# Kernel tuning notes

Measured on AMD Instinct MI355X. Metric: run time of the kernel, lower is better.

The kernel has to match this reference:

```python
import jax, jax.numpy as jnp
import numpy as np

B, N, F_IN, F_OUT = 16, 1024, 128, 128

def setup_inputs() -> dict:
    key = jax.random.key(0)
    k1, k2, k3 = jax.random.split(key, 3)
    X = jax.random.normal(k1, (B, N, F_IN), dtype=jnp.float32)
    A = jax.random.uniform(k2, (B, N, N), dtype=jnp.float32)
    W = jax.random.normal(k3, (F_IN, F_OUT), dtype=jnp.float32)
    return {"X": X, "A": A, "W": W}

def reference(X, A, W):
    # A_hat = A + I  (batched add of identity)
    n = A.shape[-1]
    A_hat = A + jnp.eye(n, dtype=A.dtype)  # [B,N,N]
    # D_hat^{-1/2} applied as elementwise row/col scaling (torch builds diag
    # matrices and inverts; mathematically identical for diagonal D).
    deg = jnp.sum(A_hat, axis=-1)               # [B,N]
    d_inv_sqrt = 1.0 / jnp.sqrt(deg)            # [B,N]
    A_norm = A_hat * d_inv_sqrt[:, :, None] * d_inv_sqrt[:, None, :]  # [B,N,N]
    out = jnp.einsum('bnm,bmf->bnf', A_norm, X)  # aggregation bmm
    out = jnp.einsum('bnf,fg->bng', out, W)      # weight matmul
    return out
```

## Files before the change

kernel.cpp:

```cpp
#include <hip/hip_runtime.h>

#define BATCH 16
#define NN 1024
#define FF 128

typedef __attribute__((ext_vector_type(8))) short bf16x8;
typedef __attribute__((ext_vector_type(4))) float f32x4;

__device__ __forceinline__ unsigned short f2bf(float x) {
  unsigned u = __float_as_uint(x);
  u += 0x7fff + ((u >> 16) & 1);
  return (unsigned short)(u >> 16);
}
__device__ __forceinline__ float bf2f(unsigned short b) {
  return __uint_as_float(((unsigned)b) << 16);
}

__global__ __launch_bounds__(256) void k_deg(const float* __restrict__ A,
                                             float* __restrict__ d) {
  int row  = blockIdx.x * 4 + (threadIdx.x >> 6);
  int lane = threadIdx.x & 63;
  const float4* Ar = (const float4*)(A + (size_t)row * NN);
  float s = 0.f;
#pragma unroll
  for (int i = 0; i < 4; ++i) {
    float4 v = Ar[lane + i * 64];
    s += (v.x + v.y) + (v.z + v.w);
  }
#pragma unroll
  for (int off = 32; off > 0; off >>= 1) s += __shfl_down(s, off, 64);
  if (lane == 0) d[row] = rsqrtf(s + 1.0f);
}

__global__ __launch_bounds__(256) void k_wt(const float* __restrict__ W,
                                            unsigned short* __restrict__ Wt) {
  int id = blockIdx.x * 256 + threadIdx.x;
  int g = id >> 7, f = id & 127;
  Wt[g * 128 + f] = f2bf(W[f * 128 + g]);
}

#define K2S 152
__global__ __launch_bounds__(256) void k_xw(const float* __restrict__ X,
                                            const unsigned short* __restrict__ Wt,
                                            const float* __restrict__ d,
                                            unsigned short* __restrict__ Yt) {
  __shared__ __align__(16) unsigned short Xl[64 * K2S];
  __shared__ __align__(16) unsigned short Wl[128 * K2S];
  __shared__ float dl[64];
  int b  = blockIdx.x >> 4;
  int m0 = (blockIdx.x & 15) * 64;
  int t  = threadIdx.x;

#pragma unroll
  for (int i = 0; i < 8; ++i) {
    int s = t + i * 256;
    int r = s >> 5, f4 = (s & 31) * 4;
    float4 v = *(const float4*)(X + ((size_t)(b * NN + m0 + r) * FF + f4));
    ushort4 p; p.x = f2bf(v.x); p.y = f2bf(v.y); p.z = f2bf(v.z); p.w = f2bf(v.w);
    *(ushort4*)(&Xl[r * K2S + f4]) = p;
  }
#pragma unroll
  for (int i = 0; i < 8; ++i) {
    int s = t + i * 256;
    int g = s >> 4, c8 = (s & 15) * 8;
    uint4 v = *(const uint4*)(Wt + (g * 128 + c8));
    *(uint4*)(&Wl[g * K2S + c8]) = v;
  }
  if (t < 64) dl[t] = d[b * NN + m0 + t];
  __syncthreads();

  int wave = t >> 6, lane = t & 63;
  int wr = wave >> 1, wc = wave & 1;
  int quad = lane >> 4, l16 = lane & 15;

  f32x4 acc[2][4];
#pragma unroll
  for (int mt = 0; mt < 2; ++mt)
#pragma unroll
    for (int ct = 0; ct < 4; ++ct) acc[mt][ct] = (f32x4){0.f, 0.f, 0.f, 0.f};

#pragma unroll
  for (int k0 = 0; k0 < 128; k0 += 32) {
    bf16x8 a[2], bb[4];
#pragma unroll
    for (int mt = 0; mt < 2; ++mt) {
      int m = wr * 32 + mt * 16 + l16;
      a[mt] = *(const bf16x8*)(&Xl[m * K2S + k0 + quad * 8]);
    }
#pragma unroll
    for (int ct = 0; ct < 4; ++ct) {
      int g = wc * 64 + ct * 16 + l16;
      bb[ct] = *(const bf16x8*)(&Wl[g * K2S + k0 + quad * 8]);
    }
#pragma unroll
    for (int mt = 0; mt < 2; ++mt)
#pragma unroll
      for (int ct = 0; ct < 4; ++ct)
        acc[mt][ct] = __builtin_amdgcn_mfma_f32_16x16x32_bf16(a[mt], bb[ct], acc[mt][ct], 0, 0, 0);
  }

#pragma unroll
  for (int mt = 0; mt < 2; ++mt) {
    int mb = wr * 32 + mt * 16 + quad * 4;
#pragma unroll
    for (int ct = 0; ct < 4; ++ct) {
      int g = wc * 64 + ct * 16 + l16;
      ushort4 p;
      p.x = f2bf(dl[mb + 0] * acc[mt][ct][0]);
      p.y = f2bf(dl[mb + 1] * acc[mt][ct][1]);
      p.z = f2bf(dl[mb + 2] * acc[mt][ct][2]);
      p.w = f2bf(dl[mb + 3] * acc[mt][ct][3]);
      *(ushort4*)(Yt + ((size_t)(b * 128 + g) * NN + m0 + mb)) = p;
    }
  }
}

#define K3S 56
__global__ __launch_bounds__(256) void k_agg(const float* __restrict__ A,
                                             const unsigned short* __restrict__ Yt,
                                             const float* __restrict__ d,
                                             float* __restrict__ out) {
  __shared__ __align__(16) unsigned short Al[32 * K3S];
  __shared__ __align__(16) unsigned short Yl[128 * K3S];
  int b  = blockIdx.x >> 5;
  int n0 = (blockIdx.x & 31) * 32;
  int t  = threadIdx.x;
  int wave = t >> 6, lane = t & 63;
  int wr = wave >> 1, wc = wave & 1;
  int quad = lane >> 4, l16 = lane & 15;

  int ar = t >> 3, ac4 = (t & 7) * 4;
  const float* Ap = A + ((size_t)(b * NN + n0 + ar) * NN + ac4);
  int yg0 = t >> 2,         yc0 = (t & 3) * 8;
  int yg1 = (t + 256) >> 2, yc1 = ((t + 256) & 3) * 8;
  const unsigned short* Yp0 = Yt + ((size_t)(b * 128 + yg0) * NN + yc0);
  const unsigned short* Yp1 = Yt + ((size_t)(b * 128 + yg1) * NN + yc1);

  f32x4 acc[4];
#pragma unroll
  for (int ct = 0; ct < 4; ++ct) acc[ct] = (f32x4){0.f, 0.f, 0.f, 0.f};

  float4 av = *(const float4*)(Ap);
  uint4 yv0 = *(const uint4*)(Yp0);
  uint4 yv1 = *(const uint4*)(Yp1);

  for (int k0 = 0; k0 < NN; k0 += 32) {
    __syncthreads();
    ushort4 ap; ap.x = f2bf(av.x); ap.y = f2bf(av.y); ap.z = f2bf(av.z); ap.w = f2bf(av.w);
    *(ushort4*)(&Al[ar * K3S + ac4]) = ap;
    *(uint4*)(&Yl[yg0 * K3S + yc0]) = yv0;
    *(uint4*)(&Yl[yg1 * K3S + yc1]) = yv1;
    __syncthreads();

    if (k0 + 32 < NN) {
      av  = *(const float4*)(Ap  + k0 + 32);
      yv0 = *(const uint4*)(Yp0 + k0 + 32);
      yv1 = *(const uint4*)(Yp1 + k0 + 32);
    }

    bf16x8 af = *(const bf16x8*)(&Al[(wr * 16 + l16) * K3S + quad * 8]);
#pragma unroll
    for (int ct = 0; ct < 4; ++ct) {
      bf16x8 bf = *(const bf16x8*)(&Yl[(wc * 64 + ct * 16 + l16) * K3S + quad * 8]);
      acc[ct] = __builtin_amdgcn_mfma_f32_16x16x32_bf16(af, bf, acc[ct], 0, 0, 0);
    }
  }

  int nb = n0 + wr * 16 + quad * 4;
  float4 d4 = *(const float4*)(d + b * NN + nb);
#pragma unroll
  for (int ct = 0; ct < 4; ++ct) {
    int g = wc * 64 + ct * 16 + l16;
    ushort4 yv = *(const ushort4*)(Yt + ((size_t)(b * 128 + g) * NN + nb));
    float* op = out + ((size_t)(b * NN + nb) * FF + g);
    op[0 * FF] = d4.x * (acc[ct][0] + bf2f(yv.x));
    op[1 * FF] = d4.y * (acc[ct][1] + bf2f(yv.y));
    op[2 * FF] = d4.z * (acc[ct][2] + bf2f(yv.z));
    op[3 * FF] = d4.w * (acc[ct][3] + bf2f(yv.w));
  }
}

extern "C" void kernel_launch(void* const* d_in, const int* in_sizes, int n_in,
                              void* d_out, int out_size, void* d_ws, size_t ws_size,
                              hipStream_t stream) {
  const float* X = (const float*)d_in[0];
  const float* A = (const float*)d_in[1];
  const float* W = (const float*)d_in[2];
  float* out = (float*)d_out;

  char* ws = (char*)d_ws;
  float*          dinv = (float*)ws;
  unsigned short* Wt   = (unsigned short*)(ws + 65536);
  unsigned short* Yt   = (unsigned short*)(ws + 65536 + 32768);

  k_deg<<<dim3(4096), dim3(256), 0, stream>>>(A, dinv);
  k_wt <<<dim3(64),   dim3(256), 0, stream>>>(W, Wt);
  k_xw <<<dim3(256),  dim3(256), 0, stream>>>(X, Wt, dinv, Yt);
  k_agg<<<dim3(512),  dim3(256), 0, stream>>>(A, Yt, dinv, out);
}
```

Before: 126.7 us.

## Drop LDS staging in xw and agg kernels, load MFMA fragments directly; fuse W transpose

Both matmul kernels now load MFMA operand fragments straight from global memory into registers instead of staging through shared memory with barriers. The aggregation kernel gives each wave an independent 16-row by 64-column tile with register double-buffering and no __syncthreads. The W transpose is folded into the degree kernel as extra blocks, removing one launch. The trade-off is that each wave reads A and Yt on its own without sharing through LDS, which means more redundant global/L2 traffic and less coalesced access patterns.

```diff
diff --git a/kernel.cpp b/kernel.cpp
--- a/kernel.cpp
+++ b/kernel.cpp
@@ -15,9 +15,25 @@
 __device__ __forceinline__ float bf2f(unsigned short b) {
   return __uint_as_float(((unsigned)b) << 16);
 }
+__device__ __forceinline__ bf16x8 cvt8(float4 a, float4 b) {
+  bf16x8 r;
+  r[0] = (short)f2bf(a.x); r[1] = (short)f2bf(a.y);
+  r[2] = (short)f2bf(a.z); r[3] = (short)f2bf(a.w);
+  r[4] = (short)f2bf(b.x); r[5] = (short)f2bf(b.y);
+  r[6] = (short)f2bf(b.z); r[7] = (short)f2bf(b.w);
+  return r;
+}
 
 __global__ __launch_bounds__(256) void k_deg(const float* __restrict__ A,
-                                             float* __restrict__ d) {
+                                             const float* __restrict__ W,
+                                             float* __restrict__ d,
+                                             unsigned short* __restrict__ Wt) {
+  if (blockIdx.x >= 4096) {
+    int id = (blockIdx.x - 4096) * 256 + threadIdx.x;
+    int g = id >> 7, f = id & 127;
+    Wt[g * 128 + f] = f2bf(W[f * 128 + g]);
+    return;
+  }
   int row  = blockIdx.x * 4 + (threadIdx.x >> 6);
   int lane = threadIdx.x & 63;
   const float4* Ar = (const float4*)(A + (size_t)row * NN);
@@ -32,146 +48,104 @@
   if (lane == 0) d[row] = rsqrtf(s + 1.0f);
 }
 
-__global__ __launch_bounds__(256) void k_wt(const float* __restrict__ W,
-                                            unsigned short* __restrict__ Wt) {
-  int id = blockIdx.x * 256 + threadIdx.x;
-  int g = id >> 7, f = id & 127;
-  Wt[g * 128 + f] = f2bf(W[f * 128 + g]);
-}
-
-#define K2S 152
 __global__ __launch_bounds__(256) void k_xw(const float* __restrict__ X,
                                             const unsigned short* __restrict__ Wt,
                                             const float* __restrict__ d,
                                             unsigned short* __restrict__ Yt) {
-  __shared__ __align__(16) unsigned short Xl[64 * K2S];
-  __shared__ __align__(16) unsigned short Wl[128 * K2S];
-  __shared__ float dl[64];
+  int t = threadIdx.x;
+  int wave = t >> 6, lane = t & 63;
+  int quad = lane >> 4, l16 = lane & 15;
   int b  = blockIdx.x >> 4;
-  int m0 = (blockIdx.x & 15) * 64;
-  int t  = threadIdx.x;
+  int m0 = ((blockIdx.x & 15) * 4 + wave) * 16;
 
+  const float* Xp = X + ((size_t)(b * NN + m0 + l16) * FF) + quad * 8;
+
+  f32x4 acc[8];
 #pragma unroll
-  for (int i = 0; i < 8; ++i) {
-    int s = t + i * 256;
-    int r = s >> 5, f4 = (s & 31) * 4;
-    float4 v = *(const float4*)(X + ((size_t)(b * NN + m0 + r) * FF + f4));
-    ushort4 p; p.x = f2bf(v.x); p.y = f2bf(v.y); p.z = f2bf(v.z); p.w = f2bf(v.w);
-    *(ushort4*)(&Xl[r * K2S + f4]) = p;
-  }
-#pragma unroll
-  for (int i = 0; i < 8; ++i) {
-    int s = t + i * 256;
-    int g = s >> 4, c8 = (s & 15) * 8;
-    uint4 v = *(const uint4*)(Wt + (g * 128 + c8));
-    *(uint4*)(&Wl[g * K2S + c8]) = v;
-  }
-  if (t < 64) dl[t] = d[b * NN + m0 + t];
-  __syncthreads();
-
-  int wave = t >> 6, lane = t & 63;
-  int wr = wave >> 1, wc = wave & 1;
-  int quad = lane >> 4, l16 = lane & 15;
-
-  f32x4 acc[2][4];
-#pragma unroll
-  for (int mt = 0; mt < 2; ++mt)
-#pragma unroll
-    for (int ct = 0; ct < 4; ++ct) acc[mt][ct] = (f32x4){0.f, 0.f, 0.f, 0.f};
+  for (int ct = 0; ct < 8; ++ct) acc[ct] = (f32x4){0.f, 0.f, 0.f, 0.f};
 
 #pragma unroll
   for (int k0 = 0; k0 < 128; k0 += 32) {
-    bf16x8 a[2], bb[4];
+    float4 a0 = *(const float4*)(Xp + k0);
+    float4 a1 = *(const float4*)(Xp + k0 + 4);
+    bf16x8 af = cvt8(a0, a1);
 #pragma unroll
-    for (int mt = 0; mt < 2; ++mt) {
-      int m = wr * 32 + mt * 16 + l16;
-      a[mt] = *(const bf16x8*)(&Xl[m * K2S + k0 + quad * 8]);
+    for (int ct = 0; ct < 8; ++ct) {
+      bf16x8 wf = *(const bf16x8*)(Wt + (ct * 16 + l16) * 128 + k0 + quad * 8);
+      acc[ct] = __builtin_amdgcn_mfma_f32_16x16x32_bf16(af, wf, acc[ct], 0, 0, 0);
     }
-#pragma unroll
-    for (int ct = 0; ct < 4; ++ct) {
-      int g = wc * 64 + ct * 16 + l16;
-      bb[ct] = *(const bf16x8*)(&Wl[g * K2S + k0 + quad * 8]);
-    }
-#pragma unroll
-    for (int mt = 0; mt < 2; ++mt)
-#pragma unroll
-      for (int ct = 0; ct < 4; ++ct)
-        acc[mt][ct] = __builtin_amdgcn_mfma_f32_16x16x32_bf16(a[mt], bb[ct], acc[mt][ct], 0, 0, 0);
   }
 
+  int mb = m0 + quad * 4;
+  float4 d4 = *(const float4*)(d + b * NN + mb);
 #pragma unroll
-  for (int mt = 0; mt < 2; ++mt) {
-    int mb = wr * 32 + mt * 16 + quad * 4;
-#pragma unroll
-    for (int ct = 0; ct < 4; ++ct) {
-      int g = wc * 64 + ct * 16 + l16;
-      ushort4 p;
-      p.x = f2bf(dl[mb + 0] * acc[mt][ct][0]);
-      p.y = f2bf(dl[mb + 1] * acc[mt][ct][1]);
-      p.z = f2bf(dl[mb + 2] * acc[mt][ct][2]);
-      p.w = f2bf(dl[mb + 3] * acc[mt][ct][3]);
-      *(ushort4*)(Yt + ((size_t)(b * 128 + g) * NN + m0 + mb)) = p;
-    }
+  for (int ct = 0; ct < 8; ++ct) {
+    int g = ct * 16 + l16;
+    ushort4 p;
+    p.x = f2bf(d4.x * acc[ct][0]);
+    p.y = f2bf(d4.y * acc[ct][1]);
+    p.z = f2bf(d4.z * acc[ct][2]);
+    p.w = f2bf(d4.w * acc[ct][3]);
+    *(ushort4*)(Yt + (size_t)(b * 128 + g) * NN + mb) = p;
   }
 }
 
-#define K3S 56
-__global__ __launch_bounds__(256) void k_agg(const float* __restrict__ A,
-                                             const unsigned short* __restrict__ Yt,
-                                             const float* __restrict__ d,
-                                             float* __restrict__ out) {
-  __shared__ __align__(16) unsigned short Al[32 * K3S];
-  __shared__ __align__(16) unsigned short Yl[128 * K3S];
-  int b  = blockIdx.x >> 5;
-  int n0 = (blockIdx.x & 31) * 32;
-  int t  = threadIdx.x;
+__global__ __launch_bounds__(256, 2) void k_agg(const float* __restrict__ A,
+                                                const unsigned short* __restrict__ Yt,
+                                                const float* __restrict__ d,
+                                                float* __restrict__ out) {
+  int t = threadIdx.x;
   int wave = t >> 6, lane = t & 63;
-  int wr = wave >> 1, wc = wave & 1;
   int quad = lane >> 4, l16 = lane & 15;
+  int b   = blockIdx.x >> 5;
+  int rem = blockIdx.x & 31;
+  int ntile = rem * 2 + (wave >> 1);
+  int gh    = wave & 1;
+  int n0 = ntile * 16;
+  int g0 = gh * 64;
 
-  int ar = t >> 3, ac4 = (t & 7) * 4;
-  const float* Ap = A + ((size_t)(b * NN + n0 + ar) * NN + ac4);
-  int yg0 = t >> 2,         yc0 = (t & 3) * 8;
-  int yg1 = (t + 256) >> 2, yc1 = ((t + 256) & 3) * 8;
-  const unsigned short* Yp0 = Yt + ((size_t)(b * 128 + yg0) * NN + yc0);
-  const unsigned short* Yp1 = Yt + ((size_t)(b * 128 + yg1) * NN + yc1);
+  const float* Ap = A + (size_t)(b * NN + n0 + l16) * NN + quad * 8;
+  const unsigned short* Yp[4];
+#pragma unroll
+  for (int ct = 0; ct < 4; ++ct)
+    Yp[ct] = Yt + (size_t)(b * 128 + g0 + ct * 16 + l16) * NN + quad * 8;
 
   f32x4 acc[4];
 #pragma unroll
   for (int ct = 0; ct < 4; ++ct) acc[ct] = (f32x4){0.f, 0.f, 0.f, 0.f};
 
-  float4 av = *(const float4*)(Ap);
-  uint4 yv0 = *(const uint4*)(Yp0);
-  uint4 yv1 = *(const uint4*)(Yp1);
+  float4 a0 = *(const float4*)(Ap);
+  float4 a1 = *(const float4*)(Ap + 4);
+  bf16x8 y[4];
+#pragma unroll
+  for (int ct = 0; ct < 4; ++ct) y[ct] = *(const bf16x8*)(Yp[ct]);
 
+#pragma unroll 2
   for (int k0 = 0; k0 < NN; k0 += 32) {
-    __syncthreads();
-    ushort4 ap; ap.x = f2bf(av.x); ap.y = f2bf(av.y); ap.z = f2bf(av.z); ap.w = f2bf(av.w);
-    *(ushort4*)(&Al[ar * K3S + ac4]) = ap;
-    *(uint4*)(&Yl[yg0 * K3S + yc0]) = yv0;
-    *(uint4*)(&Yl[yg1 * K3S + yc1]) = yv1;
-    __syncthreads();
-
+    float4 na0, na1;
+    bf16x8 ny[4];
     if (k0 + 32 < NN) {
-      av  = *(const float4*)(Ap  + k0 + 32);
-      yv0 = *(const uint4*)(Yp0 + k0 + 32);
-      yv1 = *(const uint4*)(Yp1 + k0 + 32);
+      na0 = *(const float4*)(Ap + k0 + 32);
+      na1 = *(const float4*)(Ap + k0 + 36);
+#pragma unroll
+      for (int ct = 0; ct < 4; ++ct)
+        ny[ct] = *(const bf16x8*)(Yp[ct] + k0 + 32);
     }
-
-    bf16x8 af = *(const bf16x8*)(&Al[(wr * 16 + l16) * K3S + quad * 8]);
+    bf16x8 af = cvt8(a0, a1);
 #pragma unroll
-    for (int ct = 0; ct < 4; ++ct) {
-      bf16x8 bf = *(const bf16x8*)(&Yl[(wc * 64 + ct * 16 + l16) * K3S + quad * 8]);
-      acc[ct] = __builtin_amdgcn_mfma_f32_16x16x32_bf16(af, bf, acc[ct], 0, 0, 0);
-    }
+    for (int ct = 0; ct < 4; ++ct)
+      acc[ct] = __builtin_amdgcn_mfma_f32_16x16x32_bf16(af, y[ct], acc[ct], 0, 0, 0);
+    a0 = na0; a1 = na1;
+#pragma unroll
+    for (int ct = 0; ct < 4; ++ct) y[ct] = ny[ct];
   }
 
-  int nb = n0 + wr * 16 + quad * 4;
+  int nb = n0 + quad * 4;
   float4 d4 = *(const float4*)(d + b * NN + nb);
 #pragma unroll
   for (int ct = 0; ct < 4; ++ct) {
-    int g = wc * 64 + ct * 16 + l16;
-    ushort4 yv = *(const ushort4*)(Yt + ((size_t)(b * 128 + g) * NN + nb));
+    int g = g0 + ct * 16 + l16;
+    ushort4 yv = *(const ushort4*)(Yt + (size_t)(b * 128 + g) * NN + nb);
     float* op = out + ((size_t)(b * NN + nb) * FF + g);
     op[0 * FF] = d4.x * (acc[ct][0] + bf2f(yv.x));
     op[1 * FF] = d4.y * (acc[ct][1] + bf2f(yv.y));
@@ -193,8 +167,7 @@
   unsigned short* Wt   = (unsigned short*)(ws + 65536);
   unsigned short* Yt   = (unsigned short*)(ws + 65536 + 32768);
 
-  k_deg<<<dim3(4096), dim3(256), 0, stream>>>(A, dinv);
-  k_wt <<<dim3(64),   dim3(256), 0, stream>>>(W, Wt);
-  k_xw <<<dim3(256),  dim3(256), 0, stream>>>(X, Wt, dinv, Yt);
-  k_agg<<<dim3(512),  dim3(256), 0, stream>>>(A, Yt, dinv, out);
+  k_deg<<<dim3(4096 + 64), dim3(256), 0, stream>>>(A, W, dinv, Wt);
+  k_xw <<<dim3(256),       dim3(256), 0, stream>>>(X, Wt, dinv, Yt);
+  k_agg<<<dim3(512),       dim3(256), 0, stream>>>(A, Yt, dinv, out);
 }
```

New measurement: 149.2 us. +17.8%, slower.
